# Optimization experiments

Hardware: AMD Instinct MI355X
Metric: run time of the kernel (lower is better)

The kernel has to match this reference:

```python
import jax, jax.numpy as jnp
import numpy as np

B, D, S = 8, 128, 4096

def setup_inputs() -> dict:
    key = jax.random.key(0)
    ks = jax.random.split(key, 7)
    sd = 1.0 / np.sqrt(D)
    return {
        "x": jax.random.normal(ks[0], (B, D, S), dtype=jnp.float32),
        "Wq": jax.random.normal(ks[1], (D, D), dtype=jnp.float32) * sd,
        "bq": jax.random.normal(ks[2], (D,), dtype=jnp.float32) * sd,
        "Wk": jax.random.normal(ks[3], (D, D), dtype=jnp.float32) * sd,
        "bk": jax.random.normal(ks[4], (D,), dtype=jnp.float32) * sd,
        "Wv": jax.random.normal(ks[5], (D, D), dtype=jnp.float32) * sd,
        "bv": jax.random.normal(ks[6], (D,), dtype=jnp.float32) * sd,
    }

def reference(x, Wq, bq, Wk, bk, Wv, bv):
    # x: (B, D, S) -> (B, S, D)
    xt = jnp.transpose(x, (0, 2, 1))
    scale = jnp.asarray(D, xt.dtype) ** 0.5
    # torch Linear: y = x @ W.T + b
    Q = jnp.einsum('bsd,ed->bse', xt, Wq) + bq
    K = jnp.einsum('bsd,ed->bse', xt, Wk) + bk
    V = jnp.einsum('bsd,ed->bse', xt, Wv) + bv
    scores = jnp.einsum('bqd,bkd->bqk', Q, K) / scale  # (B, S, S)
    attn = jax.nn.softmax(scores, axis=-1)
    attended = jnp.einsum('bqk,bkd->bqd', attn, V)
    out = xt + attended  # residual
    return jnp.transpose(out, (0, 2, 1))  # back to (B, D, S)
```

## Files before the change

kernel.cpp:

```cpp
#include <hip/hip_runtime.h>
#include <hip/hip_bf16.h>

#define B_ 8
#define D_ 128
#define S_ 4096

typedef short short8 __attribute__((ext_vector_type(8)));
typedef float f32x4  __attribute__((ext_vector_type(4)));
typedef float f32x16 __attribute__((ext_vector_type(16)));
typedef unsigned int uint;
typedef uint uint4v __attribute__((ext_vector_type(4)));

#define EXP2F(x) exp2f(x)

__device__ __forceinline__ short f2bf(float f) {
    __hip_bfloat16 h = __float2bfloat16(f);
    return *reinterpret_cast<short*>(&h);
}

__device__ __forceinline__ uint cvtpk(float lo, float hi) {
    uint r;
    asm("v_cvt_pk_bf16_f32 %0, %1, %2" : "=v"(r) : "v"(lo), "v"(hi));
    return r;
}

__device__ __forceinline__ void gload16(const void* g, void* l) {
    __builtin_amdgcn_global_load_lds(
        (const __attribute__((address_space(1))) void*)g,
        (__attribute__((address_space(3))) void*)l, 16, 0, 0);
}

__device__ __forceinline__ float max3f(float a, float b, float c) {
    return fmaxf(fmaxf(a, b), c);
}

__global__ __launch_bounds__(256) void wpack_kernel(
    const float* __restrict__ Wq, const float* __restrict__ Wk,
    const float* __restrict__ Wv, short* __restrict__ Wf)
{
    int g = blockIdx.x * 256 + threadIdx.x;
    int lane = g & 63, kc = (g >> 6) & 3, n = (g >> 8) & 7, wm = g >> 11;
    const float* W = (wm == 0) ? Wq : (wm == 1) ? Wk : Wv;
    int row = n * 16 + (lane & 15);
    int col = kc * 32 + (lane >> 4) * 8;
    short8 o;
    #pragma unroll
    for (int j = 0; j < 8; ++j) o[j] = f2bf(W[row * 128 + col + j]);
    *((short8*)Wf + g) = o;
}

__global__ __launch_bounds__(256) void qkv_kernel(
    const float* __restrict__ x, const short* __restrict__ Wf,
    const float* __restrict__ bq, const float* __restrict__ bk,
    const float* __restrict__ bv,
    short* __restrict__ Qo, short* __restrict__ Ko, short* __restrict__ Vo)
{
    __shared__ float xt[64 * 132];
    const int b  = blockIdx.y;
    const int s0 = blockIdx.x * 64;
    const int t  = threadIdx.x;
    const int w    = t >> 6;
    const int lane = t & 63;
    const int lr   = lane & 15;
    const int lg   = lane >> 4;

    const float* xb = x + (size_t)b * D_ * S_;
    #pragma unroll
    for (int it = 0; it < 32; ++it) {
        int d = it * 4 + (t >> 6);
        int s = t & 63;
        xt[s * 132 + d] = xb[(size_t)d * S_ + s0 + s];
    }
    __syncthreads();

    short8 xtf[4];
    {
        const float* base = &xt[(w * 16 + lr) * 132 + lg * 8];
        #pragma unroll
        for (int kc = 0; kc < 4; ++kc) {
            float4 a = *(const float4*)(base + kc * 32);
            float4 c = *(const float4*)(base + kc * 32 + 4);
            short8 f;
            f[0] = f2bf(a.x); f[1] = f2bf(a.y); f[2] = f2bf(a.z); f[3] = f2bf(a.w);
            f[4] = f2bf(c.x); f[5] = f2bf(c.y); f[6] = f2bf(c.z); f[7] = f2bf(c.w);
            xtf[kc] = f;
        }
    }

    const float qs = 0.08838834764831845f * 1.4426950408889634f;
    const short8* W8 = (const short8*)Wf;
    const size_t bSD = (size_t)b * S_ * D_;
    const size_t bDS = (size_t)b * D_ * S_;

    #pragma unroll
    for (int n = 0; n < 8; ++n) {
        f32x4 aq = (f32x4){0.f, 0.f, 0.f, 0.f};
        f32x4 ak = (f32x4){0.f, 0.f, 0.f, 0.f};
        f32x4 av = (f32x4){0.f, 0.f, 0.f, 0.f};
        #pragma unroll
        for (int kc = 0; kc < 4; ++kc) {
            short8 wq = W8[(      n * 4 + kc) * 64 + lane];
            short8 wk = W8[(32  + n * 4 + kc) * 64 + lane];
            short8 wv = W8[(64  + n * 4 + kc) * 64 + lane];
            aq = __builtin_amdgcn_mfma_f32_16x16x32_bf16(xtf[kc], wq, aq, 0, 0, 0);
            ak = __builtin_amdgcn_mfma_f32_16x16x32_bf16(xtf[kc], wk, ak, 0, 0, 0);
            av = __builtin_amdgcn_mfma_f32_16x16x32_bf16(wv, xtf[kc], av, 0, 0, 0);
        }
        int e = n * 16 + lr;
        float bqe = bq[e], bke = bk[e];
        #pragma unroll
        for (int r = 0; r < 4; ++r) {
            size_t off = (bSD + (size_t)(s0 + w * 16 + lg * 4 + r) * D_) + e;
            Qo[off] = f2bf((aq[r] + bqe) * qs);
            Ko[off] = f2bf(ak[r] + bke);
        }
        #pragma unroll
        for (int r = 0; r < 4; ++r) {
            int ev = n * 16 + lg * 4 + r;
            Vo[bDS + (size_t)ev * S_ + s0 + w * 16 + lr] = f2bf(av[r] + bv[ev]);
        }
    }
}

__global__ __launch_bounds__(512, 2) void attn_kernel(
    const short* __restrict__ Q, const short* __restrict__ K,
    const short* __restrict__ Vt, const float* __restrict__ x,
    float* __restrict__ out)
{
    extern __shared__ __align__(16) char smem[];
    const int lin = blockIdx.x;
    const int b   = lin & 7;
    const int q0  = (lin >> 3) * 128;
    const int tid  = threadIdx.x;
    const int w    = tid >> 6;
    const int lane = tid & 63;
    const int q    = lane & 31;
    const int hi   = lane >> 5;
    const int half = w >> 2;
    const int ww   = w & 3;

    const size_t bSD = (size_t)b * S_ * D_;

    short8 qf[8];
    {
        const short* Qrow = Q + bSD + (size_t)(q0 + ww * 32 + q) * D_ + hi * 8;
        #pragma unroll
        for (int c = 0; c < 8; ++c)
            qf[c] = *(const short8*)(Qrow + c * 16);
    }

    f32x16 o[4];
    #pragma unroll
    for (int dt = 0; dt < 4; ++dt)
        #pragma unroll
        for (int i = 0; i < 16; ++i) o[dt][i] = 0.f;
    float m = -1e30f, lsum = 0.f;

    const short* Kb = K + bSD;
    const short* Vb = Vt + (size_t)b * D_ * S_;
    const int ktbase = half * 32;

    auto stage = [&](int kt, int buf) {
        const short* Kg = Kb + (size_t)(ktbase + kt) * 64 * D_;
        const short* Vg = Vb + (size_t)(ktbase + kt) * 64;
        char* Kd = smem + buf * 65536 + half * 32768;
        char* Vd = Kd + 16384;
        #pragma unroll
        for (int i = 0; i < 4; ++i) {
            int ki = ww * 4 + i;
            int r  = ki * 4 + (lane >> 4);
            gload16(Kg + r * D_ + (((lane & 15) ^ (r & 7)) * 8), Kd + ki * 1024);
        }
        #pragma unroll
        for (int i = 0; i < 4; ++i) {
            int vi = ww * 4 + i;
            int r  = vi * 8 + (lane >> 3);
            gload16(Vg + (size_t)r * S_ + (((lane & 7) ^ (lane >> 3)) * 8),
                    Vd + vi * 1024);
        }
    };

    stage(0, 0);
    __syncthreads();
    int cur = 0;

    for (int kt = 0; kt < 32; ++kt) {
        if (kt + 1 < 32) stage(kt + 1, cur ^ 1);

        const char* Kh = smem + cur * 65536 + half * 32768;
        const char* Vh = Kh + 16384;

        f32x16 acc0, acc1;
        #pragma unroll
        for (int i = 0; i < 16; ++i) { acc0[i] = 0.f; acc1[i] = 0.f; }
        short8 kf[3][2];
        {
            int co0 = ((0 + hi) ^ (q & 7)) * 16;
            int co1 = ((2 + hi) ^ (q & 7)) * 16;
            kf[0][0] = *(const short8*)(Kh + q * 256 + co0);
            kf[0][1] = *(const short8*)(Kh + (32 + q) * 256 + co0);
            kf[1][0] = *(const short8*)(Kh + q * 256 + co1);
            kf[1][1] = *(const short8*)(Kh + (32 + q) * 256 + co1);
        }
        __builtin_amdgcn_s_setprio(1);
        #pragma unroll
        for (int c = 0; c < 8; ++c) {
            if (c < 6) {
                int co = (((c + 2) * 2 + hi) ^ (q & 7)) * 16;
                kf[(c + 2) % 3][0] = *(const short8*)(Kh + q * 256 + co);
                kf[(c + 2) % 3][1] = *(const short8*)(Kh + (32 + q) * 256 + co);
            }
            acc0 = __builtin_amdgcn_mfma_f32_32x32x16_bf16(kf[c % 3][0], qf[c], acc0, 0, 0, 0);
            acc1 = __builtin_amdgcn_mfma_f32_32x32x16_bf16(kf[c % 3][1], qf[c], acc1, 0, 0, 0);
        }
        __builtin_amdgcn_s_setprio(0);

        float a0 = max3f(acc0[0],  acc0[1],  acc0[2]);
        float a1 = max3f(acc0[3],  acc0[4],  acc0[5]);
        float a2 = max3f(acc0[6],  acc0[7],  acc0[8]);
        float a3 = max3f(acc0[9],  acc0[10], acc0[11]);
        float a4 = max3f(acc0[12], acc0[13], acc0[14]);
        float a5 = max3f(acc1[0],  acc1[1],  acc1[2]);
        float a6 = max3f(acc1[3],  acc1[4],  acc1[5]);
        float a7 = max3f(acc1[6],  acc1[7],  acc1[8]);
        float a8 = max3f(acc1[9],  acc1[10], acc1[11]);
        float a9 = max3f(acc1[12], acc1[13], acc1[14]);
        float b0 = max3f(a0, a1, a2);
        float b1 = max3f(a3, a4, acc0[15]);
        float b2 = max3f(a5, a6, a7);
        float b3 = max3f(a8, a9, acc1[15]);
        float tm = fmaxf(max3f(b0, b1, b2), b3);
        tm = fmaxf(tm, __shfl_xor(tm, 32));
        if (!__all(tm <= m + 8.f)) {
            float mn   = fmaxf(m, tm);
            float corr = EXP2F(m - mn);
            m = mn; lsum *= corr;
            #pragma unroll
            for (int dt = 0; dt < 4; ++dt)
                #pragma unroll
                for (int r = 0; r < 16; ++r) o[dt][r] *= corr;
        }
        #pragma unroll
        for (int r = 0; r < 16; ++r) acc0[r] = EXP2F(acc0[r] - m);
        #pragma unroll
        for (int r = 0; r < 16; ++r) acc1[r] = EXP2F(acc1[r] - m);

        short8 pf[4];
        #pragma unroll
        for (int kc = 0; kc < 4; ++kc) {
            const f32x16& a = (kc < 2) ? acc0 : acc1;
            int c1 = (kc & 1) * 8;
            uint W0 = cvtpk(a[c1 + 0], a[c1 + 1]);
            uint W1 = cvtpk(a[c1 + 2], a[c1 + 3]);
            uint W2 = cvtpk(a[c1 + 4], a[c1 + 5]);
            uint W3 = cvtpk(a[c1 + 6], a[c1 + 7]);
            asm("v_permlane32_swap_b32 %0, %1" : "+v"(W0), "+v"(W2));
            asm("v_permlane32_swap_b32 %0, %1" : "+v"(W1), "+v"(W3));
            uint4v pw;
            pw.x = W0; pw.y = W1; pw.z = W2; pw.w = W3;
            pf[kc] = *reinterpret_cast<short8*>(&pw);
        }

        short8 vf[3][2];
        {
            int co0 = ((0 + hi) ^ (q & 7)) * 16;
            vf[0][0] = *(const short8*)(Vh + (0 * 32 + q) * 128 + co0);
            vf[0][1] = *(const short8*)(Vh + (1 * 32 + q) * 128 + co0);
            vf[1][0] = *(const short8*)(Vh + (2 * 32 + q) * 128 + co0);
            vf[1][1] = *(const short8*)(Vh + (3 * 32 + q) * 128 + co0);
        }
        float s0 = ((acc0[0]+acc0[1])+(acc0[2]+acc0[3]))
                 + ((acc0[4]+acc0[5])+(acc0[6]+acc0[7]));
        float s1 = ((acc0[8]+acc0[9])+(acc0[10]+acc0[11]))
                 + ((acc0[12]+acc0[13])+(acc0[14]+acc0[15]));
        float s2 = ((acc1[0]+acc1[1])+(acc1[2]+acc1[3]))
                 + ((acc1[4]+acc1[5])+(acc1[6]+acc1[7]));
        float s3 = ((acc1[8]+acc1[9])+(acc1[10]+acc1[11]))
                 + ((acc1[12]+acc1[13])+(acc1[14]+acc1[15]));
        lsum += (s0 + s1) + (s2 + s3);

        __builtin_amdgcn_s_setprio(1);
        #pragma unroll
        for (int s = 0; s < 8; ++s) {
            if (s < 6) {
                int i0 = 2 * s + 4, i1 = 2 * s + 5;
                int coA = (((i0 >> 2) * 2 + hi) ^ (q & 7)) * 16;
                int coB = (((i1 >> 2) * 2 + hi) ^ (q & 7)) * 16;
                vf[(s + 2) % 3][0] = *(const short8*)(Vh + ((i0 & 3) * 32 + q) * 128 + coA);
                vf[(s + 2) % 3][1] = *(const short8*)(Vh + ((i1 & 3) * 32 + q) * 128 + coB);
            }
            o[(2 * s) & 3] = __builtin_amdgcn_mfma_f32_32x32x16_bf16(
                vf[s % 3][0], pf[(2 * s) >> 2], o[(2 * s) & 3], 0, 0, 0);
            o[(2 * s + 1) & 3] = __builtin_amdgcn_mfma_f32_32x32x16_bf16(
                vf[s % 3][1], pf[(2 * s + 1) >> 2], o[(2 * s + 1) & 3], 0, 0, 0);
        }
        __builtin_amdgcn_s_setprio(0);

        __syncthreads();
        cur ^= 1;
    }

    lsum += __shfl_xor(lsum, 32);

    if (half == 1) {
        float* obuf = (float*)(smem + ww * 16384);
        #pragma unroll
        for (int dt = 0; dt < 4; ++dt)
            #pragma unroll
            for (int r = 0; r < 16; ++r) {
                int dl = dt * 32 + (r & 3) + 8 * (r >> 2) + 4 * hi;
                obuf[dl * 32 + q] = o[dt][r];
            }
        if (hi == 0) {
            float* ml = (float*)(smem + 65536 + ww * 256);
            ml[q * 2]     = m;
            ml[q * 2 + 1] = lsum;
        }
    }
    __syncthreads();
    if (half == 0) {
        const float* obuf = (const float*)(smem + ww * 16384);
        const float* ml   = (const float*)(smem + 65536 + ww * 256);
        float m2 = ml[q * 2], l2 = ml[q * 2 + 1];
        float M  = fmaxf(m, m2);
        float c1 = EXP2F(m - M), c2 = EXP2F(m2 - M);
        float inv = 1.0f / (lsum * c1 + l2 * c2);
        const float* xb = x   + (size_t)b * D_ * S_;
        float*       ob = out + (size_t)b * D_ * S_;
        int s = q0 + ww * 32 + q;
        #pragma unroll
        for (int dt = 0; dt < 4; ++dt)
            #pragma unroll
            for (int r = 0; r < 16; ++r) {
                int dl = dt * 32 + (r & 3) + 8 * (r >> 2) + 4 * hi;
                float val = (o[dt][r] * c1 + obuf[dl * 32 + q] * c2) * inv;
                size_t g = (size_t)dl * S_ + s;
                ob[g] = xb[g] + val;
            }
    }
}

extern "C" void kernel_launch(void* const* d_in, const int* in_sizes, int n_in,
                              void* d_out, int out_size, void* d_ws, size_t ws_size,
                              hipStream_t stream) {
    const float* x  = (const float*)d_in[0];
    const float* Wq = (const float*)d_in[1];
    const float* bq = (const float*)d_in[2];
    const float* Wk = (const float*)d_in[3];
    const float* bk = (const float*)d_in[4];
    const float* Wv = (const float*)d_in[5];
    const float* bv = (const float*)d_in[6];
    float* out = (float*)d_out;

    size_t n = (size_t)B_ * S_ * D_;
    short* Qw = (short*)d_ws;
    short* Kw = Qw + n;
    short* Vw = Kw + n;
    short* Wf = (short*)d_out;

    wpack_kernel<<<24, 256, 0, stream>>>(Wq, Wk, Wv, Wf);

    dim3 grid(S_ / 64, B_);
    qkv_kernel<<<grid, 256, 0, stream>>>(x, Wf, bq, bk, bv, Qw, Kw, Vw);

    int smemB = 131072;
    (void)hipFuncSetAttribute((const void*)attn_kernel,
                              hipFuncAttributeMaxDynamicSharedMemorySize, smemB);
    attn_kernel<<<256, 512, smemB, stream>>>(Qw, Kw, Vw, x, out);
}
```

Before: 118.3 us.

## Stagger the two wave halves so QK MFMA overlaps softmax and PV

Restructures the attention main loop so the second half of the workgroup runs one tile behind in phase. It computes QK^T for tile t while finishing the softmax and PV of tile t-1, whereas the first half keeps the original order. This is meant to let one half's MFMA work overlap the other half's softmax VALU work on the same CU. To keep the lagging V tile alive, V staging moves to a triple buffer while K stays double-buffered, which raises LDS use to 160 KB. The cost is extra register pressure from accumulators carried across the barrier, plus more LDS.

Result: slower. 121.8 us (+3.0%).

```diff
diff --git a/kernel.cpp b/kernel.cpp
--- a/kernel.cpp
+++ b/kernel.cpp
@@ -160,11 +160,18 @@
     const short* Vb = Vt + (size_t)b * D_ * S_;
     const int ktbase = half * 32;
 
-    auto stage = [&](int kt, int buf) {
+    auto KH = [&](int t) -> const char* {
+        return smem + ((t & 1) * 2 + half) * 16384;
+    };
+    auto VH = [&](int t) -> const char* {
+        return smem + 65536 + ((t % 3) * 2 + half) * 16384;
+    };
+
+    auto stage = [&](int kt) {
         const short* Kg = Kb + (size_t)(ktbase + kt) * 64 * D_;
         const short* Vg = Vb + (size_t)(ktbase + kt) * 64;
-        char* Kd = smem + buf * 65536 + half * 32768;
-        char* Vd = Kd + 16384;
+        char* Kd = smem + ((kt & 1) * 2 + half) * 16384;
+        char* Vd = smem + 65536 + ((kt % 3) * 2 + half) * 16384;
         #pragma unroll
         for (int i = 0; i < 4; ++i) {
             int ki = ww * 4 + i;
@@ -180,17 +187,7 @@
         }
     };
 
-    stage(0, 0);
-    __syncthreads();
-    int cur = 0;
-
-    for (int kt = 0; kt < 32; ++kt) {
-        if (kt + 1 < 32) stage(kt + 1, cur ^ 1);
-
-        const char* Kh = smem + cur * 65536 + half * 32768;
-        const char* Vh = Kh + 16384;
-
-        f32x16 acc0, acc1;
+    auto qkrun = [&](const char* Kh, f32x16& acc0, f32x16& acc1) {
         #pragma unroll
         for (int i = 0; i < 16; ++i) { acc0[i] = 0.f; acc1[i] = 0.f; }
         short8 kf[3][2];
@@ -214,7 +211,9 @@
             acc1 = __builtin_amdgcn_mfma_f32_32x32x16_bf16(kf[c % 3][1], qf[c], acc1, 0, 0, 0);
         }
         __builtin_amdgcn_s_setprio(0);
-
+    };
+
+    auto finish = [&](f32x16& acc0, f32x16& acc1, const char* Vh) {
         float a0 = max3f(acc0[0],  acc0[1],  acc0[2]);
         float a1 = max3f(acc0[3],  acc0[4],  acc0[5]);
         float a2 = max3f(acc0[6],  acc0[7],  acc0[8]);
@@ -295,9 +294,31 @@
                 vf[s % 3][1], pf[(2 * s + 1) >> 2], o[(2 * s + 1) & 3], 0, 0, 0);
         }
         __builtin_amdgcn_s_setprio(0);
-
+    };
+
+    f32x16 acc0, acc1;
+
+    stage(0);
+    __syncthreads();
+
+    if (half == 0) {
+        for (int t = 0; t < 32; ++t) {
+            if (t < 31) stage(t + 1);
+            qkrun(KH(t), acc0, acc1);
+            finish(acc0, acc1, VH(t));
+            __syncthreads();
+        }
+    } else {
+        stage(1);
+        qkrun(KH(0), acc0, acc1);
         __syncthreads();
-        cur ^= 1;
+        for (int t = 1; t < 32; ++t) {
+            if (t < 31) stage(t + 1);
+            finish(acc0, acc1, VH(t - 1));
+            qkrun(KH(t), acc0, acc1);
+            __syncthreads();
+        }
+        finish(acc0, acc1, VH(31));
     }
 
     lsum += __shfl_xor(lsum, 32);
@@ -363,7 +384,7 @@
     dim3 grid(S_ / 64, B_);
     qkv_kernel<<<grid, 256, 0, stream>>>(x, Wf, bq, bk, bv, Qw, Kw, Vw);
 
-    int smemB = 131072;
+    int smemB = 163840;
     (void)hipFuncSetAttribute((const void*)attn_kernel,
                               hipFuncAttributeMaxDynamicSharedMemorySize, smemB);
     attn_kernel<<<256, 512, smemB, stream>>>(Qw, Kw, Vw, x, out);
```
